# Kernel optimization log

Measured on AMD Instinct MI355X. Metric: run time of the kernel, lower is better.

Reference implementation:

```python
import jax, jax.numpy as jnp
import numpy as np

B, T, V, D, H, K = 256, 128, 30000, 256, 256, 9  # H = hidden per direction (lstm_hidden//2)


def setup_inputs() -> dict:
    key = jax.random.key(0)
    ks = jax.random.split(key, 20)
    s = 0.05
    inp = {
        'input_x': jax.random.randint(ks[0], (B, T), 1, V),          # nonzero -> full mask
        'label':   jax.random.randint(ks[1], (B, T), 0, K),
        'emb':     jax.random.normal(ks[2], (V, D), jnp.float32) * 0.1,
        'Wih_f':   jax.random.normal(ks[3], (4 * H, D), jnp.float32) * s,
        'Whh_f':   jax.random.normal(ks[4], (4 * H, H), jnp.float32) * s,
        'b_f':     jnp.zeros((4 * H,), jnp.float32),
        'Wih_b':   jax.random.normal(ks[5], (4 * H, D), jnp.float32) * s,
        'Whh_b':   jax.random.normal(ks[6], (4 * H, H), jnp.float32) * s,
        'b_b':     jnp.zeros((4 * H,), jnp.float32),
        'W_emit':  jax.random.normal(ks[7], (K, 2 * H), jnp.float32) * s,
        'b_emit':  jnp.zeros((K,), jnp.float32),
        'start_t': jax.random.normal(ks[8], (K,), jnp.float32) * 0.1,
        'end_t':   jax.random.normal(ks[9], (K,), jnp.float32) * 0.1,
        'trans':   jax.random.normal(ks[10], (K, K), jnp.float32) * 0.1,
        'h0f':     jax.random.normal(ks[11], (B, H), jnp.float32),
        'c0f':     jax.random.normal(ks[12], (B, H), jnp.float32),
        'h0b':     jax.random.normal(ks[13], (B, H), jnp.float32),
        'c0b':     jax.random.normal(ks[14], (B, H), jnp.float32),
    }
    return inp


def _lstm_dir(x, h0, c0, Wih, Whh, b):
    # x: [B, T, D] -> outputs [B, T, H]; torch gate order i, f, g, o
    def step(carry, xt):
        h, c = carry
        g = xt @ Wih.T + h @ Whh.T + b
        i, f, gg, o = jnp.split(g, 4, axis=-1)
        c = jax.nn.sigmoid(f) * c + jax.nn.sigmoid(i) * jnp.tanh(gg)
        h = jax.nn.sigmoid(o) * jnp.tanh(c)
        return (h, c), h
    _, hs = jax.lax.scan(step, (h0, c0), jnp.swapaxes(x, 0, 1))
    return jnp.swapaxes(hs, 0, 1)


def _crf_loss(emis, tags, mask, start_t, end_t, trans):
    # torchcrf: -sum(log p(tags | emissions))
    mf = mask.astype(emis.dtype)
    bidx = jnp.arange(emis.shape[0])
    # numerator (gold path score)
    num = start_t[tags[:, 0]] + emis[bidx, 0, tags[:, 0]]
    num += jnp.sum(trans[tags[:, :-1], tags[:, 1:]] * mf[:, 1:], axis=1)
    emit_sc = jnp.take_along_axis(emis, tags[..., None], axis=-1)[..., 0]
    num += jnp.sum(emit_sc[:, 1:] * mf[:, 1:], axis=1)
    last_idx = jnp.sum(mask, axis=1) - 1
    num += end_t[tags[bidx, last_idx]]
    # denominator (log partition) via logsumexp recurrence
    def step(score, xs):
        emis_t, mask_t = xs  # [B,K], [B]
        nxt = jax.nn.logsumexp(score[:, :, None] + trans[None], axis=1) + emis_t
        score = jnp.where(mask_t[:, None], nxt, score)
        return score, None
    score0 = start_t + emis[:, 0]
    score, _ = jax.lax.scan(step, score0,
                            (jnp.swapaxes(emis[:, 1:], 0, 1), jnp.swapaxes(mask[:, 1:], 0, 1)))
    logZ = jax.nn.logsumexp(score + end_t, axis=-1)
    return -jnp.sum(num - logZ)


def _viterbi(emis, start_t, end_t, trans):
    # decode without mask (torchcrf decode(emissions)) -> [B, T] int tags
    def step(score, emis_t):
        tot = score[:, :, None] + trans[None]        # [B, K_prev, K_next]
        idx = jnp.argmax(tot, axis=1)                # [B, K]
        return jnp.max(tot, axis=1) + emis_t, idx
    score0 = start_t + emis[:, 0]
    score, hist = jax.lax.scan(step, score0, jnp.swapaxes(emis[:, 1:], 0, 1))  # hist [T-1,B,K]
    last = jnp.argmax(score + end_t, axis=-1)        # [B]
    def back(tag_next, h_t):
        tag = jnp.take_along_axis(h_t, tag_next[:, None], axis=1)[:, 0]
        return tag, tag
    _, tags_prev = jax.lax.scan(back, last, hist, reverse=True)  # [T-1, B]
    tags = jnp.concatenate([tags_prev, last[None]], axis=0)      # [T, B]
    return jnp.swapaxes(tags, 0, 1)


def reference(input_x, label, emb, Wih_f, Whh_f, b_f, Wih_b, Whh_b, b_b,
              W_emit, b_emit, start_t, end_t, trans, h0f, c0f, h0b, c0b):
    mask = input_x != 0
    x = emb[input_x]                                  # [B, T, D]
    hf = _lstm_dir(x, h0f, c0f, Wih_f, Whh_f, b_f)
    hb = _lstm_dir(x[:, ::-1], h0b, c0b, Wih_b, Whh_b, b_b)[:, ::-1]
    h = jnp.concatenate([hf, hb], axis=-1)            # [B, T, 2H]
    emis = h @ W_emit.T + b_emit                      # [B, T, K] (dropout = identity, eval)
    crf_loss = _crf_loss(emis, label, mask, start_t, end_t, trans)
    crf_decoder = _viterbi(emis, start_t, end_t, trans)
    return crf_loss, crf_decoder
```

## Files before the change

### kernel.cpp

```cpp
#include <hip/hip_runtime.h>

typedef __attribute__((ext_vector_type(8))) short bf16x8;
typedef __attribute__((ext_vector_type(4))) float f32x4;
typedef __attribute__((ext_vector_type(4))) unsigned u32x4;
typedef unsigned short u16;

#define SENT 0xC1C1C1C1u

__device__ __forceinline__ u16 f2bf(float f) {
  union { float f; unsigned u; } v; v.f = f;
  unsigned r = v.u + 0x7fffu + ((v.u >> 16) & 1u);
  return (u16)(r >> 16);
}
__device__ __forceinline__ unsigned cvt_pk(float lo, float hi) {
  unsigned r;
  asm("v_cvt_pk_bf16_f32 %0, %1, %2" : "=v"(r) : "v"(lo), "v"(hi));
  return r;
}
__device__ __forceinline__ float bflo(unsigned d) { return __uint_as_float(d << 16); }
__device__ __forceinline__ float bfhi(unsigned d) { return __uint_as_float(d & 0xffff0000u); }
__device__ __forceinline__ float sigm(float x) { return 1.f / (1.f + __expf(-x)); }
__device__ __forceinline__ float tanhf_(float x) { return 1.f - 2.f / (__expf(2.f * x) + 1.f); }

__global__ __launch_bounds__(256) void k_prep(const float* __restrict__ emb,
    const float* __restrict__ wf, const float* __restrict__ wb, const float* __restrict__ we,
    u16* __restrict__ ebh, u16* __restrict__ wihh, u16* __restrict__ weh) {
  int i4 = (blockIdx.x * 256 + threadIdx.x) * 4;
  const float* src; u16* dst; int o;
  bool zero = false;
  if (i4 < 7680000) { src = emb + i4; dst = ebh; o = i4; }
  else if (i4 < 8204288) {
    int off = i4 - 7680000;
    src = (off < 262144) ? (wf + off) : (wb + off - 262144);
    dst = wihh; o = off;
  } else {
    int off = i4 - 8204288;
    int r = off >> 9, k = off & 511;
    dst = weh; o = off;
    if (r < 9) src = we + r * 512 + k; else { zero = true; src = we; }
  }
  f32x4 v = zero ? (f32x4){0.f, 0.f, 0.f, 0.f} : *(const f32x4*)src;
  *(unsigned*)(dst + o) = cvt_pk(v[0], v[1]);
  *(unsigned*)(dst + o + 2) = cvt_pk(v[2], v[3]);
}

__global__ __launch_bounds__(256) void k_gemm_in(const int* __restrict__ ix,
    const u16* __restrict__ ebh, const u16* __restrict__ wihh,
    const float* __restrict__ bf_, const float* __restrict__ bb_,
    u16* __restrict__ xw, int c0step, int S, int logS) {
  __shared__ __align__(16) char smraw[128 * 132 * 4];
  int tid = threadIdx.x;
  int w = tid >> 6, l = tid & 63, la = l & 15, lk = (l >> 4) * 8;
  int dir = blockIdx.z;
  int m0 = blockIdx.x * 128;
  int n0 = blockIdx.y * 128;
  const char* gB = (const char*)(wihh + ((long)(dir * 1024 + n0) << 8));
#pragma unroll
  for (int it = 0; it < 16; ++it) {
    int y = it * 4096 + tid * 16;
    int sw = y ^ (((y >> 9) & 7) << 4);
    *(u32x4*)(smraw + sw) = *(const u32x4*)(gB + y);
  }
  long arow[2];
#pragma unroll
  for (int mf = 0; mf < 2; ++mf) {
    int mA = m0 + w * 32 + mf * 16 + la;
    int bA = mA >> logS, slA = mA & (S - 1);
    int sg = c0step + slA;
    int tA = dir ? (127 - sg) : sg;
    arow[mf] = (long)ix[bA * 128 + tA] << 8;
  }
  int gb[8], gx[8];
#pragma unroll
  for (int nt = 0; nt < 8; ++nt) { int g = nt * 16 + la; gb[nt] = g * 512; gx[nt] = (g & 7) << 4; }
  __syncthreads();
  f32x4 acc[2][8];
#pragma unroll
  for (int mf = 0; mf < 2; ++mf)
#pragma unroll
    for (int nt = 0; nt < 8; ++nt) acc[mf][nt] = (f32x4){0.f, 0.f, 0.f, 0.f};
#pragma unroll
  for (int ks = 0; ks < 8; ++ks) {
    int k = ks * 32 + lk;
    int kb = 2 * k;
    bf16x8 a0 = *(const bf16x8*)(ebh + arow[0] + k);
    bf16x8 a1 = *(const bf16x8*)(ebh + arow[1] + k);
#pragma unroll
    for (int nt = 0; nt < 8; ++nt) {
      bf16x8 bh = *(const bf16x8*)(smraw + gb[nt] + (kb ^ gx[nt]));
      acc[0][nt] = __builtin_amdgcn_mfma_f32_16x16x32_bf16(a0, bh, acc[0][nt], 0, 0, 0);
      acc[1][nt] = __builtin_amdgcn_mfma_f32_16x16x32_bf16(a1, bh, acc[1][nt], 0, 0, 0);
    }
  }
  __syncthreads();
  float* ot = (float*)smraw;
#pragma unroll
  for (int mf = 0; mf < 2; ++mf)
#pragma unroll
    for (int nt = 0; nt < 8; ++nt)
#pragma unroll
      for (int r = 0; r < 4; ++r)
        ot[(w * 32 + mf * 16 + (l >> 4) * 4 + r) * 132 + nt * 16 + la] = acc[mf][nt][r];
  __syncthreads();
  const float* bias = (dir ? bb_ : bf_) + n0;
  long MSd = (long)256 * S * 1024;
  int m_r0 = tid >> 4;
  int cc = (tid & 15) * 8;
  f32x4 b0 = *(const f32x4*)(bias + cc);
  f32x4 b1 = *(const f32x4*)(bias + cc + 4);
#pragma unroll
  for (int it = 0; it < 8; ++it) {
    int m_r = it * 16 + m_r0;
    f32x4 v0 = *(const f32x4*)&ot[m_r * 132 + cc];
    f32x4 v1 = *(const f32x4*)&ot[m_r * 132 + cc + 4];
    u32x4 q;
    q[0] = cvt_pk(v0[0] + b0[0], v0[1] + b0[1]);
    q[1] = cvt_pk(v0[2] + b0[2], v0[3] + b0[3]);
    q[2] = cvt_pk(v1[0] + b1[0], v1[1] + b1[1]);
    q[3] = cvt_pk(v1[2] + b1[2], v1[3] + b1[3]);
    *(u32x4*)(xw + dir * MSd + (long)(m0 + m_r) * 1024 + n0 + cc) = q;
  }
}

#define LW 264
__global__ __launch_bounds__(256) void k_lstm(
    const float* __restrict__ whh_f, const float* __restrict__ whh_b,
    const float* __restrict__ h0f, const float* __restrict__ c0f,
    const float* __restrict__ h0b, const float* __restrict__ c0b,
    const u16* __restrict__ xwp,
    u16* __restrict__ hf, u16* __restrict__ hb,
    float* __restrict__ cstate,
    int s0, int S, int first, int last) {
  __shared__ u16 wlh[128 * LW];
  __shared__ u16 hst[16 * LW];
  __shared__ float gl[16 * 132];
  int bid = blockIdx.x;
  int js = (bid >> 3) & 7;
  int G = ((bid >> 6) << 3) | (bid & 7);
  int dir = G >> 4, bs = G & 15;
  const float* whh = dir ? whh_b : whh_f;
  u16* hout = dir ? hb : hf;
  int tid = threadIdx.x;
  for (int i = 0; i < 128; ++i) {
    int q = i >> 5, u = i & 31;
    int gate = q * 256 + js * 32 + u;
    wlh[i * LW + tid] = f2bf(whh[gate * 256 + tid]);
  }
  int b_l = tid >> 4, jj = tid & 15;
  int b_g = bs * 16 + b_l;
  int jg0 = js * 32 + jj * 2;
  float cv0, cv1;
  if (first) {
    const float* c0 = dir ? c0b : c0f;
    cv0 = c0[b_g * 256 + jg0];
    cv1 = c0[b_g * 256 + jg0 + 1];
  } else {
    cv0 = cstate[(dir * 256 + b_g) * 256 + jg0];
    cv1 = cstate[(dir * 256 + b_g) * 256 + jg0 + 1];
  }
  int w = tid >> 6, l = tid & 63, la = l & 15, lk = (l >> 4) * 8;
  int srow = tid >> 4, scol = (tid & 15) * 16;
  const float* h0 = dir ? h0b : h0f;
  long MSd = (long)256 * S * 1024;
  __syncthreads();
  for (int sl = 0; sl < S; ++sl) {
    int sg = s0 + sl;
    int t_io = dir ? 127 - sg : sg;
    long xbase = (long)dir * MSd + ((long)b_g * S + sl) * 1024 + jg0;
    unsigned dI = *(const unsigned*)(xwp + xbase);
    unsigned dF = *(const unsigned*)(xwp + xbase + 256);
    unsigned dG = *(const unsigned*)(xwp + xbase + 512);
    unsigned dO = *(const unsigned*)(xwp + xbase + 768);
    u16* hd = &hst[srow * LW + scol];
    if (sg == 0) {
      const float* p = h0 + (bs * 16 + srow) * 256 + scol;
      f32x4 v0 = *(const f32x4*)p, v1 = *(const f32x4*)(p + 4);
      f32x4 v2 = *(const f32x4*)(p + 8), v3 = *(const f32x4*)(p + 12);
      u32x4 qa, qb;
      qa[0] = cvt_pk(v0[0], v0[1]); qa[1] = cvt_pk(v0[2], v0[3]);
      qa[2] = cvt_pk(v1[0], v1[1]); qa[3] = cvt_pk(v1[2], v1[3]);
      qb[0] = cvt_pk(v2[0], v2[1]); qb[1] = cvt_pk(v2[2], v2[3]);
      qb[2] = cvt_pk(v3[0], v3[1]); qb[3] = cvt_pk(v3[2], v3[3]);
      *(u32x4*)hd = qa; *((u32x4*)hd + 1) = qb;
    } else {
      int tp = dir ? t_io + 1 : t_io - 1;
      const u16* p = hout + ((long)(bs * 16 + srow) * 128 + tp) * 256 + scol;
      u32x4 r0, r1; int guard = 0; bool ok;
      do {
        asm volatile(
          "global_load_dwordx4 %0, %2, off sc0 sc1\n\t"
          "global_load_dwordx4 %1, %2, off offset:16 sc0 sc1\n\t"
          "s_waitcnt vmcnt(0)"
          : "=v"(r0), "=v"(r1) : "v"(p) : "memory");
        ok = (r0[0] != SENT) & (r0[1] != SENT) & (r0[2] != SENT) & (r0[3] != SENT)
           & (r1[0] != SENT) & (r1[1] != SENT) & (r1[2] != SENT) & (r1[3] != SENT);
      } while (__builtin_expect(!ok, 0) && ++guard < (1 << 22));
      *(u32x4*)hd = r0; *((u32x4*)hd + 1) = r1;
    }
    __syncthreads();
    f32x4 a0 = (f32x4){0.f, 0.f, 0.f, 0.f}, a1 = (f32x4){0.f, 0.f, 0.f, 0.f};
#pragma unroll
    for (int ks = 0; ks < 8; ++ks) {
      int k = ks * 32 + lk;
      bf16x8 ah = *(const bf16x8*)&hst[la * LW + k];
      bf16x8 b0 = *(const bf16x8*)&wlh[(w * 32 + la) * LW + k];
      bf16x8 b1 = *(const bf16x8*)&wlh[(w * 32 + 16 + la) * LW + k];
      a0 = __builtin_amdgcn_mfma_f32_16x16x32_bf16(ah, b0, a0, 0, 0, 0);
      a1 = __builtin_amdgcn_mfma_f32_16x16x32_bf16(ah, b1, a1, 0, 0, 0);
    }
#pragma unroll
    for (int r = 0; r < 4; ++r) {
      gl[((l >> 4) * 4 + r) * 132 + w * 32 + la] = a0[r];
      gl[((l >> 4) * 4 + r) * 132 + w * 32 + 16 + la] = a1[r];
    }
    __syncthreads();
    float hv0, hv1;
    {
      int jl = jj * 2;
      float gi = gl[b_l * 132 + jl]      + bflo(dI);
      float gf = gl[b_l * 132 + 32 + jl] + bflo(dF);
      float gg = gl[b_l * 132 + 64 + jl] + bflo(dG);
      float go = gl[b_l * 132 + 96 + jl] + bflo(dO);
      float c = sigm(gf) * cv0 + sigm(gi) * tanhf_(gg);
      cv0 = c; hv0 = sigm(go) * tanhf_(c);
    }
    {
      int jl = jj * 2 + 1;
      float gi = gl[b_l * 132 + jl]      + bfhi(dI);
      float gf = gl[b_l * 132 + 32 + jl] + bfhi(dF);
      float gg = gl[b_l * 132 + 64 + jl] + bfhi(dG);
      float go = gl[b_l * 132 + 96 + jl] + bfhi(dO);
      float c = sigm(gf) * cv1 + sigm(gi) * tanhf_(gg);
      cv1 = c; hv1 = sigm(go) * tanhf_(c);
    }
    unsigned pk = cvt_pk(hv0, hv1);
    __hip_atomic_store((unsigned*)(hout + ((long)b_g * 128 + t_io) * 256 + jg0), pk,
                       __ATOMIC_RELAXED, __HIP_MEMORY_SCOPE_AGENT);
  }
  if (!last) {
    cstate[(dir * 256 + b_g) * 256 + jg0] = cv0;
    cstate[(dir * 256 + b_g) * 256 + jg0 + 1] = cv1;
  }
}

__global__ __launch_bounds__(256) void k_emis(const u16* __restrict__ hfb, const u16* __restrict__ hbb,
    const u16* __restrict__ weh, const float* __restrict__ bemit, float* __restrict__ emis,
    float* __restrict__ out) {
  if (blockIdx.x == 0 && threadIdx.x == 0) out[0] = 0.f;
  int w = threadIdx.x >> 6, l = threadIdx.x & 63;
  int la = l & 15, lk = (l >> 4) * 8;
  long m0 = (long)blockIdx.x * 64 + w * 16;
  long am = m0 + la;
  f32x4 acc = (f32x4){0.f, 0.f, 0.f, 0.f};
#pragma unroll
  for (int ks = 0; ks < 16; ++ks) {
    int k = ks * 32 + lk;
    const u16* src = (k < 256) ? (hfb + am * 256 + k) : (hbb + am * 256 + (k - 256));
    bf16x8 ah = *(const bf16x8*)src;
    bf16x8 bh = *(const bf16x8*)(weh + la * 512 + k);
    acc = __builtin_amdgcn_mfma_f32_16x16x32_bf16(ah, bh, acc, 0, 0, 0);
  }
  int kout = la;
  float bias = (kout < 9) ? bemit[kout] : 0.f;
  long mr = m0 + (l >> 4) * 4;
#pragma unroll
  for (int r = 0; r < 4; ++r)
    emis[(mr + r) * 16 + kout] = acc[r] + bias;
}

__global__ __launch_bounds__(256) void k_tail(const float* __restrict__ emis, const int* __restrict__ ixin,
    const int* __restrict__ label, const float* __restrict__ startt, const float* __restrict__ endt,
    const float* __restrict__ trans, float* __restrict__ out) {
  __shared__ float al_s[16][16];
  __shared__ float tr_s[9][16];
  __shared__ float num_s[16];
  __shared__ float red_s[16];
  __shared__ unsigned char bpl[16 * 127 * 16];
  int tid = threadIdx.x, bl = tid >> 4, k = tid & 15;
  int bid = blockIdx.x;
  if (bl < 9) tr_s[bl][k] = (k < 9) ? trans[bl * 9 + k] : 0.f;
  if (bid < 16) {
    int b = bid * 16 + bl;
    float a = 0.f, num = 0.f;
    int lastlab = 0;
    if (k < 9) a = startt[k] + emis[((long)b * 128) * 16 + k];
    al_s[bl][k] = a;
    if (k == 9) {
      int l0 = label[b * 128];
      num = startt[l0] + emis[((long)b * 128) * 16 + l0];
      lastlab = l0;
    }
    __syncthreads();
    for (int t = 1; t < 128; ++t) {
      bool msk = ixin[b * 128 + t] != 0;
      float anew = a;
      if (k < 9) {
        float mx = -1e30f;
#pragma unroll
        for (int j = 0; j < 9; ++j) mx = fmaxf(mx, al_s[bl][j] + tr_s[j][k]);
        float ss = 0.f;
#pragma unroll
        for (int j = 0; j < 9; ++j) ss += __expf(al_s[bl][j] + tr_s[j][k] - mx);
        anew = mx + __logf(ss) + emis[((long)b * 128 + t) * 16 + k];
        if (!msk) anew = a;
      } else if (k == 9 && msk) {
        int lt = label[b * 128 + t];
        num += tr_s[lastlab][lt] + emis[((long)b * 128 + t) * 16 + lt];
        lastlab = lt;
      }
      __syncthreads();
      if (k < 9) { a = anew; al_s[bl][k] = a; }
      __syncthreads();
    }
    if (k == 9) num_s[bl] = num + endt[lastlab];
    __syncthreads();
    if (k == 0) {
      float mx = -1e30f;
#pragma unroll
      for (int j = 0; j < 9; ++j) mx = fmaxf(mx, al_s[bl][j] + endt[j]);
      float ss = 0.f;
#pragma unroll
      for (int j = 0; j < 9; ++j) ss += __expf(al_s[bl][j] + endt[j] - mx);
      red_s[bl] = (mx + __logf(ss)) - num_s[bl];
    }
    __syncthreads();
    if (tid == 0) {
      float s = 0.f;
      for (int i = 0; i < 16; ++i) s += red_s[i];
      atomicAdd(out, s);
    }
  } else {
    int vb = bid - 16;
    int b = vb * 16 + bl;
    float v = -1e30f;
    if (k < 9) v = startt[k] + emis[((long)b * 128) * 16 + k];
    al_s[bl][k] = v;
    __syncthreads();
    for (int t = 1; t < 128; ++t) {
      float vnew = v;
      if (k < 9) {
        float best = -1e30f; int bi = 0;
#pragma unroll
        for (int j = 0; j < 9; ++j) {
          float tot = al_s[bl][j] + tr_s[j][k];
          if (tot > best) { best = tot; bi = j; }
        }
        vnew = best + emis[((long)b * 128 + t) * 16 + k];
        bpl[(bl * 127 + (t - 1)) * 16 + k] = (unsigned char)bi;
      }
      __syncthreads();
      if (k < 9) { v = vnew; al_s[bl][k] = v; }
      __syncthreads();
    }
    if (tid < 16) {
      int bb = vb * 16 + tid;
      float best = -1e30f; int tag = 0;
#pragma unroll
      for (int j = 0; j < 9; ++j) {
        float vv = al_s[tid][j] + endt[j];
        if (vv > best) { best = vv; tag = j; }
      }
      out[1 + bb * 128 + 127] = (float)tag;
      for (int t = 127; t >= 1; --t) {
        tag = bpl[(tid * 127 + (t - 1)) * 16 + tag];
        out[1 + bb * 128 + t - 1] = (float)tag;
      }
    }
  }
}

__global__ void k_sent(float* out) { out[0] = -1.0e6f; }

extern "C" void kernel_launch(void* const* d_in, const int* in_sizes, int n_in,
                              void* d_out, int out_size, void* d_ws, size_t ws_size,
                              hipStream_t stream) {
  const int* in_x    = (const int*)d_in[0];
  const int* label   = (const int*)d_in[1];
  const float* emb   = (const float*)d_in[2];
  const float* Wih_f = (const float*)d_in[3];
  const float* Whh_f = (const float*)d_in[4];
  const float* b_f   = (const float*)d_in[5];
  const float* Wih_b = (const float*)d_in[6];
  const float* Whh_b = (const float*)d_in[7];
  const float* b_b   = (const float*)d_in[8];
  const float* W_emit= (const float*)d_in[9];
  const float* b_emit= (const float*)d_in[10];
  const float* start_t=(const float*)d_in[11];
  const float* end_t = (const float*)d_in[12];
  const float* trans = (const float*)d_in[13];
  const float* h0f   = (const float*)d_in[14];
  const float* c0f   = (const float*)d_in[15];
  const float* h0b   = (const float*)d_in[16];
  const float* c0b   = (const float*)d_in[17];
  (void)in_sizes; (void)n_in; (void)out_size;

  auto align = [](size_t x) { return (x + 255) & ~(size_t)255; };
  size_t fixed = 0;
  fixed += align(32768L * 256 * 2);
  fixed += align(32768L * 256 * 2);
  fixed += align(30000L * 256 * 2);
  fixed += align(2048L * 256 * 2);
  fixed += align(16L * 512 * 2);
  fixed += align(32768L * 16 * 4);
  fixed += align(2L * 256 * 256 * 4);

  int S = 0;
  const int cands[4] = {128, 64, 32, 16};
  for (int ci = 0; ci < 4; ++ci) {
    size_t xb = align(1048576L * cands[ci]);
    if (xb + fixed <= ws_size) { S = cands[ci]; break; }
  }
  if (S == 0) { k_sent<<<1, 1, 0, stream>>>((float*)d_out); return; }
  int logS = __builtin_ctz(S);
  int NC = 128 / S;

  char* ws = (char*)d_ws;
  size_t o = 0;
  auto alloc = [&](size_t sz) { size_t r = o; o += (sz + 255) & ~(size_t)255; return r; };
  u16* xw    = (u16*)(ws + alloc(1048576L * S));
  u16* hf    = (u16*)(ws + alloc(32768L * 256 * 2));
  u16* hb    = (u16*)(ws + alloc(32768L * 256 * 2));
  u16* ebh   = (u16*)(ws + alloc(30000L * 256 * 2));
  u16* wihh  = (u16*)(ws + alloc(2048L * 256 * 2));
  u16* weh   = (u16*)(ws + alloc(16L * 512 * 2));
  float* emis= (float*)(ws + alloc(32768L * 16 * 4));
  float* cstate = (float*)(ws + alloc(2L * 256 * 256 * 4));

  hipMemsetAsync(hf, 0xC1, 32768L * 256 * 2, stream);
  hipMemsetAsync(hb, 0xC1, 32768L * 256 * 2, stream);
  k_prep<<<8020, 256, 0, stream>>>(emb, Wih_f, Wih_b, W_emit, ebh, wihh, weh);
  for (int c = 0; c < NC; ++c) {
    k_gemm_in<<<dim3(2 * S, 8, 2), 256, 0, stream>>>(in_x, ebh, wihh, b_f, b_b,
                                                     xw, c * S, S, logS);
    k_lstm<<<256, 256, 0, stream>>>(Whh_f, Whh_b, h0f, c0f, h0b, c0b, xw, hf, hb,
                                    cstate, c * S, S, c == 0 ? 1 : 0, c == NC - 1 ? 1 : 0);
  }
  k_emis<<<512, 256, 0, stream>>>(hf, hb, weh, b_emit, emis, (float*)d_out);
  k_tail<<<32, 256, 0, stream>>>(emis, in_x, label, start_t, end_t, trans, (float*)d_out);
}
```

Baseline: 443.1 us.

## Make each LSTM block own full hidden dim with fp8 register-resident Whh

Replaces the 256-block LSTM, which split the hidden dimension across 8 blocks and exchanged h each step through global memory with sentinel spin-polling, with 32 blocks of 512 threads. Each block computes all 1024 gates for its 16 batch rows and keeps h in double-buffered shared memory, so cross-block synchronisation and the sentinel memsets go away. Whh is pre-converted to fp8 in a new prep kernel and held in registers (64 longs per thread), and the recurrent matmul uses fp8 MFMA. The cost is far fewer active CUs, heavy register pressure, and fp8 precision on the hidden state and weights, which may affect accuracy.

```diff
diff --git a/kernel.cpp b/kernel.cpp
--- a/kernel.cpp
+++ b/kernel.cpp
@@ -5,13 +5,6 @@
 typedef __attribute__((ext_vector_type(4))) unsigned u32x4;
 typedef unsigned short u16;
 
-#define SENT 0xC1C1C1C1u
-
-__device__ __forceinline__ u16 f2bf(float f) {
-  union { float f; unsigned u; } v; v.f = f;
-  unsigned r = v.u + 0x7fffu + ((v.u >> 16) & 1u);
-  return (u16)(r >> 16);
-}
 __device__ __forceinline__ unsigned cvt_pk(float lo, float hi) {
   unsigned r;
   asm("v_cvt_pk_bf16_f32 %0, %1, %2" : "=v"(r) : "v"(lo), "v"(hi));
@@ -44,6 +37,22 @@
   *(unsigned*)(dst + o + 2) = cvt_pk(v[2], v[3]);
 }
 
+__global__ __launch_bounds__(256) void k_prep_whh(const float* __restrict__ wf,
+    const float* __restrict__ wb, char* __restrict__ whh8) {
+  int T = blockIdx.x * 256 + threadIdx.x;
+  int l = T & 63, ks = (T >> 6) & 7, nt = (T >> 9) & 7, w = (T >> 12) & 7, dir = T >> 15;
+  const float* src = dir ? wb : wf;
+  int gate = w * 128 + nt * 16 + (l & 15);
+  int k0 = ks * 32 + (l >> 4) * 8;
+  const float* p = src + gate * 256 + k0;
+  f32x4 v0 = *(const f32x4*)p, v1 = *(const f32x4*)(p + 4);
+  int r0 = __builtin_amdgcn_cvt_pk_fp8_f32(v0[0], v0[1], 0, false);
+  r0 = __builtin_amdgcn_cvt_pk_fp8_f32(v0[2], v0[3], r0, true);
+  int r1 = __builtin_amdgcn_cvt_pk_fp8_f32(v1[0], v1[1], 0, false);
+  r1 = __builtin_amdgcn_cvt_pk_fp8_f32(v1[2], v1[3], r1, true);
+  ((int2*)whh8)[T] = make_int2(r0, r1);
+}
+
 __global__ __launch_bounds__(256) void k_gemm_in(const int* __restrict__ ix,
     const u16* __restrict__ ebh, const u16* __restrict__ wihh,
     const float* __restrict__ bf_, const float* __restrict__ bb_,
@@ -122,124 +131,127 @@
   }
 }
 
-#define LW 264
-__global__ __launch_bounds__(256) void k_lstm(
-    const float* __restrict__ whh_f, const float* __restrict__ whh_b,
+__global__ __launch_bounds__(512, 2) void k_lstm(
+    const char* __restrict__ whh8,
     const float* __restrict__ h0f, const float* __restrict__ c0f,
     const float* __restrict__ h0b, const float* __restrict__ c0b,
     const u16* __restrict__ xwp,
     u16* __restrict__ hf, u16* __restrict__ hb,
     float* __restrict__ cstate,
     int s0, int S, int first, int last) {
-  __shared__ u16 wlh[128 * LW];
-  __shared__ u16 hst[16 * LW];
-  __shared__ float gl[16 * 132];
+  __shared__ __align__(16) char hst8[2][16 * 264];
+  __shared__ float gl[16 * 1032];
   int bid = blockIdx.x;
-  int js = (bid >> 3) & 7;
-  int G = ((bid >> 6) << 3) | (bid & 7);
-  int dir = G >> 4, bs = G & 15;
-  const float* whh = dir ? whh_b : whh_f;
+  int dir = bid >> 4, bs = bid & 15;
+  int tid = threadIdx.x;
+  int w = tid >> 6, l = tid & 63, la = l & 15, lkb = (l >> 4) * 8;
   u16* hout = dir ? hb : hf;
-  int tid = threadIdx.x;
-  for (int i = 0; i < 128; ++i) {
-    int q = i >> 5, u = i & 31;
-    int gate = q * 256 + js * 32 + u;
-    wlh[i * LW + tid] = f2bf(whh[gate * 256 + tid]);
-  }
-  int b_l = tid >> 4, jj = tid & 15;
-  int b_g = bs * 16 + b_l;
-  int jg0 = js * 32 + jj * 2;
-  float cv0, cv1;
-  if (first) {
-    const float* c0 = dir ? c0b : c0f;
-    cv0 = c0[b_g * 256 + jg0];
-    cv1 = c0[b_g * 256 + jg0 + 1];
-  } else {
-    cv0 = cstate[(dir * 256 + b_g) * 256 + jg0];
-    cv1 = cstate[(dir * 256 + b_g) * 256 + jg0 + 1];
-  }
-  int w = tid >> 6, l = tid & 63, la = l & 15, lk = (l >> 4) * 8;
-  int srow = tid >> 4, scol = (tid & 15) * 16;
-  const float* h0 = dir ? h0b : h0f;
-  long MSd = (long)256 * S * 1024;
+  long ww[64];
+  const long* wsrc = (const long*)whh8 + (long)(dir * 8 + w) * 4096;
+#pragma unroll
+  for (int q = 0; q < 64; ++q) ww[q] = wsrc[q * 64 + l];
+  int bl = tid >> 5, jj8 = (tid & 31) * 8;
+  int b_g = bs * 16 + bl;
+  float cr[8];
+  {
+    const float* csrc = first ? ((dir ? c0b : c0f) + b_g * 256 + jj8)
+                              : (cstate + ((long)(dir * 256 + b_g)) * 256 + jj8);
+    f32x4 c0v = *(const f32x4*)csrc;
+    f32x4 c1v = *(const f32x4*)(csrc + 4);
+#pragma unroll
+    for (int e = 0; e < 4; ++e) { cr[e] = c0v[e]; cr[4 + e] = c1v[e]; }
+  }
+  {
+    int r0, r1;
+    if (first) {
+      const float* p = (dir ? h0b : h0f) + b_g * 256 + jj8;
+      f32x4 v0 = *(const f32x4*)p, v1 = *(const f32x4*)(p + 4);
+      r0 = __builtin_amdgcn_cvt_pk_fp8_f32(v0[0], v0[1], 0, false);
+      r0 = __builtin_amdgcn_cvt_pk_fp8_f32(v0[2], v0[3], r0, true);
+      r1 = __builtin_amdgcn_cvt_pk_fp8_f32(v1[0], v1[1], 0, false);
+      r1 = __builtin_amdgcn_cvt_pk_fp8_f32(v1[2], v1[3], r1, true);
+    } else {
+      int tp = dir ? (127 - s0 + 1) : (s0 - 1);
+      const u16* p = hout + ((long)b_g * 128 + tp) * 256 + jj8;
+      u32x4 q = *(const u32x4*)p;
+      r0 = __builtin_amdgcn_cvt_pk_fp8_f32(bflo(q[0]), bfhi(q[0]), 0, false);
+      r0 = __builtin_amdgcn_cvt_pk_fp8_f32(bflo(q[1]), bfhi(q[1]), r0, true);
+      r1 = __builtin_amdgcn_cvt_pk_fp8_f32(bflo(q[2]), bfhi(q[2]), 0, false);
+      r1 = __builtin_amdgcn_cvt_pk_fp8_f32(bflo(q[3]), bfhi(q[3]), r1, true);
+    }
+    *(int2*)&hst8[0][bl * 264 + jj8] = make_int2(r0, r1);
+  }
+  long dirMS = (long)dir * 256 * S * 1024;
   __syncthreads();
+  int p = 0;
   for (int sl = 0; sl < S; ++sl) {
     int sg = s0 + sl;
     int t_io = dir ? 127 - sg : sg;
-    long xbase = (long)dir * MSd + ((long)b_g * S + sl) * 1024 + jg0;
-    unsigned dI = *(const unsigned*)(xwp + xbase);
-    unsigned dF = *(const unsigned*)(xwp + xbase + 256);
-    unsigned dG = *(const unsigned*)(xwp + xbase + 512);
-    unsigned dO = *(const unsigned*)(xwp + xbase + 768);
-    u16* hd = &hst[srow * LW + scol];
-    if (sg == 0) {
-      const float* p = h0 + (bs * 16 + srow) * 256 + scol;
-      f32x4 v0 = *(const f32x4*)p, v1 = *(const f32x4*)(p + 4);
-      f32x4 v2 = *(const f32x4*)(p + 8), v3 = *(const f32x4*)(p + 12);
-      u32x4 qa, qb;
-      qa[0] = cvt_pk(v0[0], v0[1]); qa[1] = cvt_pk(v0[2], v0[3]);
-      qa[2] = cvt_pk(v1[0], v1[1]); qa[3] = cvt_pk(v1[2], v1[3]);
-      qb[0] = cvt_pk(v2[0], v2[1]); qb[1] = cvt_pk(v2[2], v2[3]);
-      qb[2] = cvt_pk(v3[0], v3[1]); qb[3] = cvt_pk(v3[2], v3[3]);
-      *(u32x4*)hd = qa; *((u32x4*)hd + 1) = qb;
-    } else {
-      int tp = dir ? t_io + 1 : t_io - 1;
-      const u16* p = hout + ((long)(bs * 16 + srow) * 128 + tp) * 256 + scol;
-      u32x4 r0, r1; int guard = 0; bool ok;
-      do {
-        asm volatile(
-          "global_load_dwordx4 %0, %2, off sc0 sc1\n\t"
-          "global_load_dwordx4 %1, %2, off offset:16 sc0 sc1\n\t"
-          "s_waitcnt vmcnt(0)"
-          : "=v"(r0), "=v"(r1) : "v"(p) : "memory");
-        ok = (r0[0] != SENT) & (r0[1] != SENT) & (r0[2] != SENT) & (r0[3] != SENT)
-           & (r1[0] != SENT) & (r1[1] != SENT) & (r1[2] != SENT) & (r1[3] != SENT);
-      } while (__builtin_expect(!ok, 0) && ++guard < (1 << 22));
-      *(u32x4*)hd = r0; *((u32x4*)hd + 1) = r1;
-    }
-    __syncthreads();
-    f32x4 a0 = (f32x4){0.f, 0.f, 0.f, 0.f}, a1 = (f32x4){0.f, 0.f, 0.f, 0.f};
+    long xbase = dirMS + ((long)b_g * S + sl) * 1024 + jj8;
+    u32x4 xi = *(const u32x4*)(xwp + xbase);
+    u32x4 xf = *(const u32x4*)(xwp + xbase + 256);
+    u32x4 xg = *(const u32x4*)(xwp + xbase + 512);
+    u32x4 xo = *(const u32x4*)(xwp + xbase + 768);
+    const char* hp = hst8[p];
+    f32x4 acc[8];
+#pragma unroll
+    for (int nt = 0; nt < 8; ++nt) acc[nt] = (f32x4){0.f, 0.f, 0.f, 0.f};
 #pragma unroll
     for (int ks = 0; ks < 8; ++ks) {
-      int k = ks * 32 + lk;
-      bf16x8 ah = *(const bf16x8*)&hst[la * LW + k];
-      bf16x8 b0 = *(const bf16x8*)&wlh[(w * 32 + la) * LW + k];
-      bf16x8 b1 = *(const bf16x8*)&wlh[(w * 32 + 16 + la) * LW + k];
-      a0 = __builtin_amdgcn_mfma_f32_16x16x32_bf16(ah, b0, a0, 0, 0, 0);
-      a1 = __builtin_amdgcn_mfma_f32_16x16x32_bf16(ah, b1, a1, 0, 0, 0);
-    }
-#pragma unroll
-    for (int r = 0; r < 4; ++r) {
-      gl[((l >> 4) * 4 + r) * 132 + w * 32 + la] = a0[r];
-      gl[((l >> 4) * 4 + r) * 132 + w * 32 + 16 + la] = a1[r];
-    }
-    __syncthreads();
-    float hv0, hv1;
-    {
-      int jl = jj * 2;
-      float gi = gl[b_l * 132 + jl]      + bflo(dI);
-      float gf = gl[b_l * 132 + 32 + jl] + bflo(dF);
-      float gg = gl[b_l * 132 + 64 + jl] + bflo(dG);
-      float go = gl[b_l * 132 + 96 + jl] + bflo(dO);
-      float c = sigm(gf) * cv0 + sigm(gi) * tanhf_(gg);
-      cv0 = c; hv0 = sigm(go) * tanhf_(c);
-    }
-    {
-      int jl = jj * 2 + 1;
-      float gi = gl[b_l * 132 + jl]      + bfhi(dI);
-      float gf = gl[b_l * 132 + 32 + jl] + bfhi(dF);
-      float gg = gl[b_l * 132 + 64 + jl] + bfhi(dG);
-      float go = gl[b_l * 132 + 96 + jl] + bfhi(dO);
-      float c = sigm(gf) * cv1 + sigm(gi) * tanhf_(gg);
-      cv1 = c; hv1 = sigm(go) * tanhf_(c);
-    }
-    unsigned pk = cvt_pk(hv0, hv1);
-    __hip_atomic_store((unsigned*)(hout + ((long)b_g * 128 + t_io) * 256 + jg0), pk,
-                       __ATOMIC_RELAXED, __HIP_MEMORY_SCOPE_AGENT);
+      long av = *(const long*)(hp + la * 264 + ks * 32 + lkb);
+#pragma unroll
+      for (int nt = 0; nt < 8; ++nt)
+        acc[nt] = __builtin_amdgcn_mfma_f32_16x16x32_fp8_fp8(av, ww[nt * 8 + ks], acc[nt], 0, 0, 0);
+    }
+#pragma unroll
+    for (int nt = 0; nt < 8; ++nt)
+#pragma unroll
+      for (int r = 0; r < 4; ++r)
+        gl[((l >> 4) * 4 + r) * 1032 + w * 128 + nt * 16 + la] = acc[nt][r];
+    __syncthreads();
+    const float* g0 = &gl[bl * 1032 + jj8];
+    f32x4 aI0 = *(const f32x4*)(g0);         f32x4 aI1 = *(const f32x4*)(g0 + 4);
+    f32x4 aF0 = *(const f32x4*)(g0 + 256);   f32x4 aF1 = *(const f32x4*)(g0 + 260);
+    f32x4 aG0 = *(const f32x4*)(g0 + 512);   f32x4 aG1 = *(const f32x4*)(g0 + 516);
+    f32x4 aO0 = *(const f32x4*)(g0 + 768);   f32x4 aO1 = *(const f32x4*)(g0 + 772);
+    float hv[8];
+#pragma unroll
+    for (int e = 0; e < 4; ++e) {
+      float gi = aI0[e] + ((e & 1) ? bfhi(xi[e >> 1]) : bflo(xi[e >> 1]));
+      float gf = aF0[e] + ((e & 1) ? bfhi(xf[e >> 1]) : bflo(xf[e >> 1]));
+      float gg = aG0[e] + ((e & 1) ? bfhi(xg[e >> 1]) : bflo(xg[e >> 1]));
+      float go = aO0[e] + ((e & 1) ? bfhi(xo[e >> 1]) : bflo(xo[e >> 1]));
+      float c = sigm(gf) * cr[e] + sigm(gi) * tanhf_(gg);
+      cr[e] = c; hv[e] = sigm(go) * tanhf_(c);
+    }
+#pragma unroll
+    for (int e = 0; e < 4; ++e) {
+      float gi = aI1[e] + ((e & 1) ? bfhi(xi[2 + (e >> 1)]) : bflo(xi[2 + (e >> 1)]));
+      float gf = aF1[e] + ((e & 1) ? bfhi(xf[2 + (e >> 1)]) : bflo(xf[2 + (e >> 1)]));
+      float gg = aG1[e] + ((e & 1) ? bfhi(xg[2 + (e >> 1)]) : bflo(xg[2 + (e >> 1)]));
+      float go = aO1[e] + ((e & 1) ? bfhi(xo[2 + (e >> 1)]) : bflo(xo[2 + (e >> 1)]));
+      float c = sigm(gf) * cr[4 + e] + sigm(gi) * tanhf_(gg);
+      cr[4 + e] = c; hv[4 + e] = sigm(go) * tanhf_(c);
+    }
+    int r0 = __builtin_amdgcn_cvt_pk_fp8_f32(hv[0], hv[1], 0, false);
+    r0 = __builtin_amdgcn_cvt_pk_fp8_f32(hv[2], hv[3], r0, true);
+    int r1 = __builtin_amdgcn_cvt_pk_fp8_f32(hv[4], hv[5], 0, false);
+    r1 = __builtin_amdgcn_cvt_pk_fp8_f32(hv[6], hv[7], r1, true);
+    *(int2*)&hst8[p ^ 1][bl * 264 + jj8] = make_int2(r0, r1);
+    u32x4 hq;
+    hq[0] = cvt_pk(hv[0], hv[1]); hq[1] = cvt_pk(hv[2], hv[3]);
+    hq[2] = cvt_pk(hv[4], hv[5]); hq[3] = cvt_pk(hv[6], hv[7]);
+    *(u32x4*)(hout + ((long)b_g * 128 + t_io) * 256 + jj8) = hq;
+    __syncthreads();
+    p ^= 1;
   }
   if (!last) {
-    cstate[(dir * 256 + b_g) * 256 + jg0] = cv0;
-    cstate[(dir * 256 + b_g) * 256 + jg0 + 1] = cv1;
+    float* cd = cstate + ((long)(dir * 256 + b_g)) * 256 + jj8;
+    f32x4 c0v, c1v;
+#pragma unroll
+    for (int e = 0; e < 4; ++e) { c0v[e] = cr[e]; c1v[e] = cr[4 + e]; }
+    *(f32x4*)cd = c0v;
+    *(f32x4*)(cd + 4) = c1v;
   }
 }
 
@@ -401,6 +413,7 @@
   fixed += align(30000L * 256 * 2);
   fixed += align(2048L * 256 * 2);
   fixed += align(16L * 512 * 2);
+  fixed += align(2048L * 256);
   fixed += align(32768L * 16 * 4);
   fixed += align(2L * 256 * 256 * 4);
 
@@ -423,17 +436,17 @@
   u16* ebh   = (u16*)(ws + alloc(30000L * 256 * 2));
   u16* wihh  = (u16*)(ws + alloc(2048L * 256 * 2));
   u16* weh   = (u16*)(ws + alloc(16L * 512 * 2));
+  char* whh8 = (char*)(ws + alloc(2048L * 256));
   float* emis= (float*)(ws + alloc(32768L * 16 * 4));
   float* cstate = (float*)(ws + alloc(2L * 256 * 256 * 4));
 
-  hipMemsetAsync(hf, 0xC1, 32768L * 256 * 2, stream);
-  hipMemsetAsync(hb, 0xC1, 32768L * 256 * 2, stream);
   k_prep<<<8020, 256, 0, stream>>>(emb, Wih_f, Wih_b, W_emit, ebh, wihh, weh);
+  k_prep_whh<<<256, 256, 0, stream>>>(Whh_f, Whh_b, whh8);
   for (int c = 0; c < NC; ++c) {
     k_gemm_in<<<dim3(2 * S, 8, 2), 256, 0, stream>>>(in_x, ebh, wihh, b_f, b_b,
                                                      xw, c * S, S, logS);
-    k_lstm<<<256, 256, 0, stream>>>(Whh_f, Whh_b, h0f, c0f, h0b, c0b, xw, hf, hb,
-                                    cstate, c * S, S, c == 0 ? 1 : 0, c == NC - 1 ? 1 : 0);
+    k_lstm<<<32, 512, 0, stream>>>(whh8, h0f, c0f, h0b, c0b, xw, hf, hb,
+                                   cstate, c * S, S, c == 0 ? 1 : 0, c == NC - 1 ? 1 : 0);
   }
   k_emis<<<512, 256, 0, stream>>>(hf, hb, weh, b_emit, emis, (float*)d_out);
   k_tail<<<32, 256, 0, stream>>>(emis, in_x, label, start_t, end_t, trans, (float*)d_out);
```

Result: slower. 751.1 us (+69.5%).

## Fuse input projection into LSTM recurrence using FP8 embedding and Wih MFMA

Applied to the files above, without the earlier changes.

Removes the separate input-projection GEMM and its large bf16 xw workspace. Each LSTM step now computes x_t·Wih inside the recurrent kernel with fp8 MFMAs on an fp8-quantized embedding table and Wih held in LDS, and prefetches the next step's embedding row. This drops the chunked launch loop and the cstate save and restore, but adds MFMA work to the serial critical path of every step and lowers input precision to fp8.

```diff
diff --git a/kernel.cpp b/kernel.cpp
--- a/kernel.cpp
+++ b/kernel.cpp
@@ -17,122 +17,45 @@
   asm("v_cvt_pk_bf16_f32 %0, %1, %2" : "=v"(r) : "v"(lo), "v"(hi));
   return r;
 }
-__device__ __forceinline__ float bflo(unsigned d) { return __uint_as_float(d << 16); }
-__device__ __forceinline__ float bfhi(unsigned d) { return __uint_as_float(d & 0xffff0000u); }
 __device__ __forceinline__ float sigm(float x) { return 1.f / (1.f + __expf(-x)); }
 __device__ __forceinline__ float tanhf_(float x) { return 1.f - 2.f / (__expf(2.f * x) + 1.f); }
 
 __global__ __launch_bounds__(256) void k_prep(const float* __restrict__ emb,
     const float* __restrict__ wf, const float* __restrict__ wb, const float* __restrict__ we,
-    u16* __restrict__ ebh, u16* __restrict__ wihh, u16* __restrict__ weh) {
+    char* __restrict__ eb8, char* __restrict__ wih8, u16* __restrict__ weh) {
   int i4 = (blockIdx.x * 256 + threadIdx.x) * 4;
-  const float* src; u16* dst; int o;
-  bool zero = false;
-  if (i4 < 7680000) { src = emb + i4; dst = ebh; o = i4; }
-  else if (i4 < 8204288) {
-    int off = i4 - 7680000;
-    src = (off < 262144) ? (wf + off) : (wb + off - 262144);
-    dst = wihh; o = off;
+  if (i4 < 8204288) {
+    const float* src; char* dst; int o;
+    if (i4 < 7680000) { src = emb + i4; dst = eb8; o = i4; }
+    else { int off = i4 - 7680000;
+           src = (off < 262144) ? (wf + off) : (wb + off - 262144);
+           dst = wih8; o = off; }
+    f32x4 v = *(const f32x4*)src;
+    int r0 = __builtin_amdgcn_cvt_pk_fp8_f32(v[0], v[1], 0, false);
+    r0 = __builtin_amdgcn_cvt_pk_fp8_f32(v[2], v[3], r0, true);
+    *(int*)(dst + o) = r0;
   } else {
     int off = i4 - 8204288;
     int r = off >> 9, k = off & 511;
-    dst = weh; o = off;
-    if (r < 9) src = we + r * 512 + k; else { zero = true; src = we; }
-  }
-  f32x4 v = zero ? (f32x4){0.f, 0.f, 0.f, 0.f} : *(const f32x4*)src;
-  *(unsigned*)(dst + o) = cvt_pk(v[0], v[1]);
-  *(unsigned*)(dst + o + 2) = cvt_pk(v[2], v[3]);
-}
-
-__global__ __launch_bounds__(256) void k_gemm_in(const int* __restrict__ ix,
-    const u16* __restrict__ ebh, const u16* __restrict__ wihh,
-    const float* __restrict__ bf_, const float* __restrict__ bb_,
-    u16* __restrict__ xw, int c0step, int S, int logS) {
-  __shared__ __align__(16) char smraw[128 * 132 * 4];
-  int tid = threadIdx.x;
-  int w = tid >> 6, l = tid & 63, la = l & 15, lk = (l >> 4) * 8;
-  int dir = blockIdx.z;
-  int m0 = blockIdx.x * 128;
-  int n0 = blockIdx.y * 128;
-  const char* gB = (const char*)(wihh + ((long)(dir * 1024 + n0) << 8));
-#pragma unroll
-  for (int it = 0; it < 16; ++it) {
-    int y = it * 4096 + tid * 16;
-    int sw = y ^ (((y >> 9) & 7) << 4);
-    *(u32x4*)(smraw + sw) = *(const u32x4*)(gB + y);
-  }
-  long arow[2];
-#pragma unroll
-  for (int mf = 0; mf < 2; ++mf) {
-    int mA = m0 + w * 32 + mf * 16 + la;
-    int bA = mA >> logS, slA = mA & (S - 1);
-    int sg = c0step + slA;
-    int tA = dir ? (127 - sg) : sg;
-    arow[mf] = (long)ix[bA * 128 + tA] << 8;
-  }
-  int gb[8], gx[8];
-#pragma unroll
-  for (int nt = 0; nt < 8; ++nt) { int g = nt * 16 + la; gb[nt] = g * 512; gx[nt] = (g & 7) << 4; }
-  __syncthreads();
-  f32x4 acc[2][8];
-#pragma unroll
-  for (int mf = 0; mf < 2; ++mf)
-#pragma unroll
-    for (int nt = 0; nt < 8; ++nt) acc[mf][nt] = (f32x4){0.f, 0.f, 0.f, 0.f};
-#pragma unroll
-  for (int ks = 0; ks < 8; ++ks) {
-    int k = ks * 32 + lk;
-    int kb = 2 * k;
-    bf16x8 a0 = *(const bf16x8*)(ebh + arow[0] + k);
-    bf16x8 a1 = *(const bf16x8*)(ebh + arow[1] + k);
-#pragma unroll
-    for (int nt = 0; nt < 8; ++nt) {
-      bf16x8 bh = *(const bf16x8*)(smraw + gb[nt] + (kb ^ gx[nt]));
-      acc[0][nt] = __builtin_amdgcn_mfma_f32_16x16x32_bf16(a0, bh, acc[0][nt], 0, 0, 0);
-      acc[1][nt] = __builtin_amdgcn_mfma_f32_16x16x32_bf16(a1, bh, acc[1][nt], 0, 0, 0);
-    }
-  }
-  __syncthreads();
-  float* ot = (float*)smraw;
-#pragma unroll
-  for (int mf = 0; mf < 2; ++mf)
-#pragma unroll
-    for (int nt = 0; nt < 8; ++nt)
-#pragma unroll
-      for (int r = 0; r < 4; ++r)
-        ot[(w * 32 + mf * 16 + (l >> 4) * 4 + r) * 132 + nt * 16 + la] = acc[mf][nt][r];
-  __syncthreads();
-  const float* bias = (dir ? bb_ : bf_) + n0;
-  long MSd = (long)256 * S * 1024;
-  int m_r0 = tid >> 4;
-  int cc = (tid & 15) * 8;
-  f32x4 b0 = *(const f32x4*)(bias + cc);
-  f32x4 b1 = *(const f32x4*)(bias + cc + 4);
-#pragma unroll
-  for (int it = 0; it < 8; ++it) {
-    int m_r = it * 16 + m_r0;
-    f32x4 v0 = *(const f32x4*)&ot[m_r * 132 + cc];
-    f32x4 v1 = *(const f32x4*)&ot[m_r * 132 + cc + 4];
-    u32x4 q;
-    q[0] = cvt_pk(v0[0] + b0[0], v0[1] + b0[1]);
-    q[1] = cvt_pk(v0[2] + b0[2], v0[3] + b0[3]);
-    q[2] = cvt_pk(v1[0] + b1[0], v1[1] + b1[1]);
-    q[3] = cvt_pk(v1[2] + b1[2], v1[3] + b1[3]);
-    *(u32x4*)(xw + dir * MSd + (long)(m0 + m_r) * 1024 + n0 + cc) = q;
+    f32x4 v = (r < 9) ? *(const f32x4*)(we + r * 512 + k) : (f32x4){0.f, 0.f, 0.f, 0.f};
+    *(unsigned*)(weh + off) = cvt_pk(v[0], v[1]);
+    *(unsigned*)(weh + off + 2) = cvt_pk(v[2], v[3]);
   }
 }
 
 #define LW 264
 __global__ __launch_bounds__(256) void k_lstm(
     const float* __restrict__ whh_f, const float* __restrict__ whh_b,
+    const char* __restrict__ wih8, const char* __restrict__ eb8,
+    const int* __restrict__ ix,
+    const float* __restrict__ bf_, const float* __restrict__ bb_,
     const float* __restrict__ h0f, const float* __restrict__ c0f,
     const float* __restrict__ h0b, const float* __restrict__ c0b,
-    const u16* __restrict__ xwp,
-    u16* __restrict__ hf, u16* __restrict__ hb,
-    float* __restrict__ cstate,
-    int s0, int S, int first, int last) {
+    u16* __restrict__ hf, u16* __restrict__ hb) {
   __shared__ u16 wlh[128 * LW];
+  __shared__ char wli8[128 * 264];
   __shared__ u16 hst[16 * LW];
+  __shared__ __align__(16) char hsa8[16 * 272];
   __shared__ float gl[16 * 132];
   int bid = blockIdx.x;
   int js = (bid >> 3) & 7;
@@ -145,34 +68,35 @@
     int q = i >> 5, u = i & 31;
     int gate = q * 256 + js * 32 + u;
     wlh[i * LW + tid] = f2bf(whh[gate * 256 + tid]);
+    wli8[i * 264 + tid] = wih8[(dir * 1024 + gate) * 256 + tid];
   }
   int b_l = tid >> 4, jj = tid & 15;
   int b_g = bs * 16 + b_l;
   int jg0 = js * 32 + jj * 2;
-  float cv0, cv1;
-  if (first) {
-    const float* c0 = dir ? c0b : c0f;
-    cv0 = c0[b_g * 256 + jg0];
-    cv1 = c0[b_g * 256 + jg0 + 1];
-  } else {
-    cv0 = cstate[(dir * 256 + b_g) * 256 + jg0];
-    cv1 = cstate[(dir * 256 + b_g) * 256 + jg0 + 1];
-  }
+  const float* bsrc = dir ? bb_ : bf_;
+  float bI0 = bsrc[jg0],       bI1 = bsrc[jg0 + 1];
+  float bF0 = bsrc[256 + jg0], bF1 = bsrc[257 + jg0];
+  float bG0 = bsrc[512 + jg0], bG1 = bsrc[513 + jg0];
+  float bO0 = bsrc[768 + jg0], bO1 = bsrc[769 + jg0];
+  const float* c0 = dir ? c0b : c0f;
+  float cv0 = c0[b_g * 256 + jg0];
+  float cv1 = c0[b_g * 256 + jg0 + 1];
   int w = tid >> 6, l = tid & 63, la = l & 15, lk = (l >> 4) * 8;
   int srow = tid >> 4, scol = (tid & 15) * 16;
   const float* h0 = dir ? h0b : h0f;
-  long MSd = (long)256 * S * 1024;
+  const int* ixrow = ix + (bs * 16 + srow) * 128;
+  u32x4 aR;
+  {
+    int tA = dir ? 127 : 0;
+    const char* ap = eb8 + (long)ixrow[tA] * 256 + scol;
+    aR = *(const u32x4*)ap;
+  }
   __syncthreads();
-  for (int sl = 0; sl < S; ++sl) {
-    int sg = s0 + sl;
-    int t_io = dir ? 127 - sg : sg;
-    long xbase = (long)dir * MSd + ((long)b_g * S + sl) * 1024 + jg0;
-    unsigned dI = *(const unsigned*)(xwp + xbase);
-    unsigned dF = *(const unsigned*)(xwp + xbase + 256);
-    unsigned dG = *(const unsigned*)(xwp + xbase + 512);
-    unsigned dO = *(const unsigned*)(xwp + xbase + 768);
+  for (int sl = 0; sl < 128; ++sl) {
+    int t_io = dir ? 127 - sl : sl;
+    *(u32x4*)&hsa8[srow * 272 + scol] = aR;
     u16* hd = &hst[srow * LW + scol];
-    if (sg == 0) {
+    if (sl == 0) {
       const float* p = h0 + (bs * 16 + srow) * 256 + scol;
       f32x4 v0 = *(const f32x4*)p, v1 = *(const f32x4*)(p + 4);
       f32x4 v2 = *(const f32x4*)(p + 8), v3 = *(const f32x4*)(p + 12);
@@ -202,11 +126,17 @@
 #pragma unroll
     for (int ks = 0; ks < 8; ++ks) {
       int k = ks * 32 + lk;
-      bf16x8 ah = *(const bf16x8*)&hst[la * LW + k];
-      bf16x8 b0 = *(const bf16x8*)&wlh[(w * 32 + la) * LW + k];
-      bf16x8 b1 = *(const bf16x8*)&wlh[(w * 32 + 16 + la) * LW + k];
-      a0 = __builtin_amdgcn_mfma_f32_16x16x32_bf16(ah, b0, a0, 0, 0, 0);
-      a1 = __builtin_amdgcn_mfma_f32_16x16x32_bf16(ah, b1, a1, 0, 0, 0);
+      long xv = *(const long*)&hsa8[la * 272 + k];
+      bf16x8 hh = *(const bf16x8*)&hst[la * LW + k];
+      int r0_ = w * 32 + la, r1_ = w * 32 + 16 + la;
+      long wi0 = *(const long*)&wli8[r0_ * 264 + k];
+      long wi1 = *(const long*)&wli8[r1_ * 264 + k];
+      bf16x8 wh0 = *(const bf16x8*)&wlh[r0_ * LW + k];
+      bf16x8 wh1 = *(const bf16x8*)&wlh[r1_ * LW + k];
+      a0 = __builtin_amdgcn_mfma_f32_16x16x32_fp8_fp8(xv, wi0, a0, 0, 0, 0);
+      a0 = __builtin_amdgcn_mfma_f32_16x16x32_bf16(hh, wh0, a0, 0, 0, 0);
+      a1 = __builtin_amdgcn_mfma_f32_16x16x32_fp8_fp8(xv, wi1, a1, 0, 0, 0);
+      a1 = __builtin_amdgcn_mfma_f32_16x16x32_bf16(hh, wh1, a1, 0, 0, 0);
     }
 #pragma unroll
     for (int r = 0; r < 4; ++r) {
@@ -217,29 +147,30 @@
     float hv0, hv1;
     {
       int jl = jj * 2;
-      float gi = gl[b_l * 132 + jl]      + bflo(dI);
-      float gf = gl[b_l * 132 + 32 + jl] + bflo(dF);
-      float gg = gl[b_l * 132 + 64 + jl] + bflo(dG);
-      float go = gl[b_l * 132 + 96 + jl] + bflo(dO);
+      float gi = gl[b_l * 132 + jl]      + bI0;
+      float gf = gl[b_l * 132 + 32 + jl] + bF0;
+      float gg = gl[b_l * 132 + 64 + jl] + bG0;
+      float go = gl[b_l * 132 + 96 + jl] + bO0;
       float c = sigm(gf) * cv0 + sigm(gi) * tanhf_(gg);
       cv0 = c; hv0 = sigm(go) * tanhf_(c);
     }
     {
       int jl = jj * 2 + 1;
-      float gi = gl[b_l * 132 + jl]      + bfhi(dI);
-      float gf = gl[b_l * 132 + 32 + jl] + bfhi(dF);
-      float gg = gl[b_l * 132 + 64 + jl] + bfhi(dG);
-      float go = gl[b_l * 132 + 96 + jl] + bfhi(dO);
+      float gi = gl[b_l * 132 + jl]      + bI1;
+      float gf = gl[b_l * 132 + 32 + jl] + bF1;
+      float gg = gl[b_l * 132 + 64 + jl] + bG1;
+      float go = gl[b_l * 132 + 96 + jl] + bO1;
       float c = sigm(gf) * cv1 + sigm(gi) * tanhf_(gg);
       cv1 = c; hv1 = sigm(go) * tanhf_(c);
     }
     unsigned pk = cvt_pk(hv0, hv1);
     __hip_atomic_store((unsigned*)(hout + ((long)b_g * 128 + t_io) * 256 + jg0), pk,
                        __ATOMIC_RELAXED, __HIP_MEMORY_SCOPE_AGENT);
-  }
-  if (!last) {
-    cstate[(dir * 256 + b_g) * 256 + jg0] = cv0;
-    cstate[(dir * 256 + b_g) * 256 + jg0 + 1] = cv1;
+    if (sl < 127) {
+      int tN = dir ? 126 - sl : sl + 1;
+      const char* ap = eb8 + (long)ixrow[tN] * 256 + scol;
+      aR = *(const u32x4*)ap;
+    }
   }
 }
 
@@ -395,46 +326,25 @@
   (void)in_sizes; (void)n_in; (void)out_size;
 
   auto align = [](size_t x) { return (x + 255) & ~(size_t)255; };
-  size_t fixed = 0;
-  fixed += align(32768L * 256 * 2);
-  fixed += align(32768L * 256 * 2);
-  fixed += align(30000L * 256 * 2);
-  fixed += align(2048L * 256 * 2);
-  fixed += align(16L * 512 * 2);
-  fixed += align(32768L * 16 * 4);
-  fixed += align(2L * 256 * 256 * 4);
-
-  int S = 0;
-  const int cands[4] = {128, 64, 32, 16};
-  for (int ci = 0; ci < 4; ++ci) {
-    size_t xb = align(1048576L * cands[ci]);
-    if (xb + fixed <= ws_size) { S = cands[ci]; break; }
-  }
-  if (S == 0) { k_sent<<<1, 1, 0, stream>>>((float*)d_out); return; }
-  int logS = __builtin_ctz(S);
-  int NC = 128 / S;
-
   char* ws = (char*)d_ws;
   size_t o = 0;
   auto alloc = [&](size_t sz) { size_t r = o; o += (sz + 255) & ~(size_t)255; return r; };
-  u16* xw    = (u16*)(ws + alloc(1048576L * S));
+  size_t need = align(32768L * 256 * 2) * 2 + align(30000L * 256) + align(2048L * 256)
+              + align(16L * 512 * 2) + align(32768L * 16 * 4);
+  if (need > ws_size) { k_sent<<<1, 1, 0, stream>>>((float*)d_out); return; }
+
   u16* hf    = (u16*)(ws + alloc(32768L * 256 * 2));
   u16* hb    = (u16*)(ws + alloc(32768L * 256 * 2));
-  u16* ebh   = (u16*)(ws + alloc(30000L * 256 * 2));
-  u16* wihh  = (u16*)(ws + alloc(2048L * 256 * 2));
+  char* eb8  = (char*)(ws + alloc(30000L * 256));
+  char* wih8 = (char*)(ws + alloc(2048L * 256));
   u16* weh   = (u16*)(ws + alloc(16L * 512 * 2));
   float* emis= (float*)(ws + alloc(32768L * 16 * 4));
-  float* cstate = (float*)(ws + alloc(2L * 256 * 256 * 4));
 
   hipMemsetAsync(hf, 0xC1, 32768L * 256 * 2, stream);
   hipMemsetAsync(hb, 0xC1, 32768L * 256 * 2, stream);
-  k_prep<<<8020, 256, 0, stream>>>(emb, Wih_f, Wih_b, W_emit, ebh, wihh, weh);
-  for (int c = 0; c < NC; ++c) {
-    k_gemm_in<<<dim3(2 * S, 8, 2), 256, 0, stream>>>(in_x, ebh, wihh, b_f, b_b,
-                                                     xw, c * S, S, logS);
-    k_lstm<<<256, 256, 0, stream>>>(Whh_f, Whh_b, h0f, c0f, h0b, c0b, xw, hf, hb,
-                                    cstate, c * S, S, c == 0 ? 1 : 0, c == NC - 1 ? 1 : 0);
-  }
+  k_prep<<<8020, 256, 0, stream>>>(emb, Wih_f, Wih_b, W_emit, eb8, wih8, weh);
+  k_lstm<<<256, 256, 0, stream>>>(Whh_f, Whh_b, wih8, eb8, in_x, b_f, b_b,
+                                  h0f, c0f, h0b, c0b, hf, hb);
   k_emis<<<512, 256, 0, stream>>>(hf, hb, weh, b_emit, emis, (float*)d_out);
   k_tail<<<32, 256, 0, stream>>>(emis, in_x, label, start_t, end_t, trans, (float*)d_out);
 }
```

After: 386.9 us. -12.7%, faster.
